# Kernel optimization log

Measured on AMD Instinct MI355X. Metric: run time of the kernel, lower is better.

Reference implementation:

```python
import jax, jax.numpy as jnp
import numpy as np

GRAPH_SIZE = 512  # N: graph_size from init


def setup_inputs() -> dict:
    key = jax.random.key(0)
    k1, k2 = jax.random.split(key)
    B, N, C_IN, C_OUT = 128, GRAPH_SIZE, 128, 128
    # X packs [adjacency | features] along last dim, matching the torch forward
    X = jax.random.uniform(k1, (B, N, N + C_IN), dtype=jnp.float32)
    W = jax.random.normal(k2, (C_IN, C_OUT), dtype=jnp.float32)
    return {"X": X, "W": W}


def reference(X, W):
    N = GRAPH_SIZE
    A = X[:, :, :N]            # [B, N, N] dense adjacency
    feat = X[:, :, N:]         # [B, N, C_in]
    # D = diag(rowsum(A)); pinv(D).sqrt() == diag(1/sqrt(deg)) with 0 where deg==0
    deg = jnp.sum(A, axis=2)   # [B, N]
    d_inv_sqrt = jnp.where(deg > 0, 1.0 / jnp.sqrt(deg), 0.0)
    A_hat = A + jnp.eye(N, dtype=A.dtype)  # A + I
    # D^-1/2 @ A_hat @ D^-1/2 as elementwise row/col scaling (diag matmuls)
    A_norm = d_inv_sqrt[:, :, None] * A_hat * d_inv_sqrt[:, None, :]
    # relu(A_norm @ X @ W)
    h = jnp.einsum('bnm,bmf->bnf', A_norm, feat)
    out = jax.nn.relu(jnp.einsum('bnf,fo->bno', h, W))
    return jnp.concatenate([A, out], axis=2)  # [B, N, N + C_out]
```

## Files before the change

kernel.cpp:

```cpp
#include <hip/hip_runtime.h>
#include <stdint.h>

#define GS   512
#define CF   128
#define XROW 640
#define NB   128

typedef __attribute__((ext_vector_type(4))) float          f32x4;
typedef __attribute__((ext_vector_type(8))) short          s16x8;
typedef __attribute__((ext_vector_type(4))) unsigned short u16x4;
typedef __attribute__((ext_vector_type(8))) unsigned short u16x8;

__device__ __forceinline__ unsigned short f2bf(float f) {
    unsigned u = __builtin_bit_cast(unsigned, f);
    u = (u + 0x7fffu + ((u >> 16) & 1u)) >> 16;
    return (unsigned short)u;
}
__device__ __forceinline__ float bf2f(unsigned short h) {
    unsigned u = ((unsigned)h) << 16;
    return __builtin_bit_cast(float, u);
}
__device__ __forceinline__ void glds16(const void* g, void* l) {
    __builtin_amdgcn_global_load_lds(
        (const __attribute__((address_space(1))) void*)g,
        (__attribute__((address_space(3))) void*)l, 16, 0, 0);
}

__global__ __launch_bounds__(256) void k0_wt(const float* __restrict__ W,
                                             unsigned short* __restrict__ WTst) {
    const int e = blockIdx.x * 256 + threadIdx.x;
    const int j = e & 7, f = (e >> 3) & 127, q = e >> 10;
    const int c = (q >> 2) * 32 + (q & 3) * 8 + j;
    WTst[e] = f2bf(W[c * CF + f]);
}

__global__ __launch_bounds__(256) void k1_pre(const float* __restrict__ X,
                                              float* __restrict__ out,
                                              float* __restrict__ dis,
                                              unsigned short* __restrict__ Abf) {
    const int wv = threadIdx.x >> 6, l = threadIdx.x & 63;
    const int gbase = blockIdx.x << 3;
#pragma unroll
    for (int p = 0; p < 2; ++p) {
        const int gr = gbase + wv + (p << 2);
        const f32x4* rp = (const f32x4*)(X + (size_t)gr * XROW);
        f32x4* op = (f32x4*)(out + (size_t)gr * XROW);
        f32x4 v0 = rp[2 * l], v1 = rp[2 * l + 1];
        op[2 * l] = v0; op[2 * l + 1] = v1;
        u16x8 o;
        o[0] = f2bf(v0[0]); o[1] = f2bf(v0[1]); o[2] = f2bf(v0[2]); o[3] = f2bf(v0[3]);
        o[4] = f2bf(v1[0]); o[5] = f2bf(v1[1]); o[6] = f2bf(v1[2]); o[7] = f2bf(v1[3]);
        const int b = gr >> 9, n = gr & (GS - 1);
        const int rt = n >> 4, lr = n & 15;
        *(u16x8*)((char*)Abf + (((size_t)(b * 32 + rt)) << 14) + (l << 8) + (lr << 4)) = o;
        float s = (v0[0] + v0[1]) + (v0[2] + v0[3]) + (v1[0] + v1[1]) + (v1[2] + v1[3]);
#pragma unroll
        for (int off = 32; off; off >>= 1) s += __shfl_xor(s, off, 64);
        if (l == 0) dis[gr] = (s > 0.f) ? (1.f / sqrtf(s)) : 0.f;
    }
}

__global__ __launch_bounds__(256) void k2_featw(const float* __restrict__ X,
                                                const unsigned short* __restrict__ WTst,
                                                const float* __restrict__ dis,
                                                unsigned short* __restrict__ fwdT) {
    __shared__ __align__(16) float sf[64 * 128];
    __shared__ __align__(16) unsigned short swt[16384];
    const int t = threadIdx.x, l = t & 63, wv = t >> 6;
    const int m0 = blockIdx.x << 6;
    const int b = m0 >> 9, ml0 = m0 & (GS - 1);

    const char* fb = (const char*)(X + (size_t)m0 * XROW + GS);
    char* sfb = (char*)sf;
#pragma unroll
    for (int it = 0; it < 8; ++it) {
        int chunk = it * 256 + t;
        int row = chunk >> 5, c16 = chunk & 31;
        int c16s = c16 ^ (row & 7);
        glds16(fb + (size_t)row * (XROW * 4) + c16s * 16, sfb + it * 4096 + wv * 1024);
    }
#pragma unroll
    for (int it = 0; it < 8; ++it)
        glds16((const char*)WTst + it * 4096 + wv * 1024 + l * 16,
               (char*)swt + it * 4096 + wv * 1024);
    __syncthreads();

    const int wr = wv >> 1, wc = wv & 1, lr = l & 15, lk = l >> 4;
    f32x4 acc[2][4];
#pragma unroll
    for (int i = 0; i < 2; ++i)
#pragma unroll
        for (int j = 0; j < 4; ++j)
#pragma unroll
            for (int r = 0; r < 4; ++r) acc[i][j][r] = 0.f;

#pragma unroll
    for (int ks = 0; ks < 4; ++ks) {
        s16x8 af[2];
#pragma unroll
        for (int i = 0; i < 2; ++i) {
            int row = (wr << 5) + (i << 4) + lr;
            int cb = (ks << 3) + (lk << 1);
            int c0 = cb ^ (row & 7), c1 = (cb + 1) ^ (row & 7);
            f32x4 x0 = *(const f32x4*)&sf[row * 128 + (c0 << 2)];
            f32x4 x1 = *(const f32x4*)&sf[row * 128 + (c1 << 2)];
            s16x8 a;
            a[0] = f2bf(x0[0]); a[1] = f2bf(x0[1]); a[2] = f2bf(x0[2]); a[3] = f2bf(x0[3]);
            a[4] = f2bf(x1[0]); a[5] = f2bf(x1[1]); a[6] = f2bf(x1[2]); a[7] = f2bf(x1[3]);
            af[i] = a;
        }
#pragma unroll
        for (int j = 0; j < 4; ++j) {
            int f = (wc << 6) + (j << 4) + lr;
            s16x8 bfr = *(const s16x8*)&swt[((((ks << 2) | lk) << 7) | f) << 3];
#pragma unroll
            for (int i = 0; i < 2; ++i)
                acc[i][j] = __builtin_amdgcn_mfma_f32_16x16x32_bf16(af[i], bfr, acc[i][j], 0, 0, 0);
        }
    }

#pragma unroll
    for (int i = 0; i < 2; ++i) {
        int mr = (wr << 5) + (i << 4) + (lk << 2);
        f32x4 d4 = *(const f32x4*)&dis[m0 + mr];
        int mg = ml0 + mr;
        int ktm = mg >> 5, q3 = (mg >> 3) & 3, jm = mg & 7;
#pragma unroll
        for (int j = 0; j < 4; ++j) {
            int f = (wc << 6) + (j << 4) + lr;
            u16x4 o;
            o[0] = f2bf(d4[0] * acc[i][j][0]);
            o[1] = f2bf(d4[1] * acc[i][j][1]);
            o[2] = f2bf(d4[2] * acc[i][j][2]);
            o[3] = f2bf(d4[3] * acc[i][j][3]);
            *(u16x4*)((char*)fwdT + ((size_t)b << 17) + (((ktm << 2) | q3) << 11)
                      + (f << 4) + (jm << 1)) = o;
        }
    }
}

__global__ __launch_bounds__(256) void k3_gcn(const unsigned short* __restrict__ Abf,
                                              const float* __restrict__ dis,
                                              const unsigned short* __restrict__ fwdT,
                                              float* __restrict__ out) {
    __shared__ __align__(16) unsigned short sb[2][4096];
    const int t = threadIdx.x, l = t & 63, wv = t >> 6, lr = l & 15, lk = l >> 4;
    const int b = blockIdx.x >> 3, bm0 = (blockIdx.x & 7) << 6;
    const char* Bt = (const char*)fwdT + ((size_t)b << 17);
    const int rt = (bm0 >> 4) + wv;
    const char* Ab = (const char*)Abf + (((size_t)(b * 32 + rt)) << 14);

    auto stage = [&](int buf, int kt) {
#pragma unroll
        for (int it = 0; it < 2; ++it)
            glds16(Bt + (kt << 13) + it * 4096 + wv * 1024 + l * 16,
                   (char*)sb[buf] + it * 4096 + wv * 1024);
    };

    f32x4 acc[8];
#pragma unroll
    for (int j = 0; j < 8; ++j)
#pragma unroll
        for (int r = 0; r < 4; ++r) acc[j][r] = 0.f;

    stage(0, 0);
    s16x8 a = *(const s16x8*)(Ab + (l << 4));
    int cur = 0;
    for (int kt = 0; kt < 16; ++kt) {
        __syncthreads();
        if (kt < 15) stage(cur ^ 1, kt + 1);
        s16x8 an = a;
        if (kt < 15) an = *(const s16x8*)(Ab + ((kt + 1) << 10) + (l << 4));
#pragma unroll
        for (int j = 0; j < 8; ++j) {
            s16x8 bfr = *(const s16x8*)&sb[cur][(lk << 10) + (j << 7) + (lr << 3)];
            acc[j] = __builtin_amdgcn_mfma_f32_16x16x32_bf16(a, bfr, acc[j], 0, 0, 0);
        }
        a = an; cur ^= 1;
    }

    const int n0 = bm0 + (wv << 4) + (lk << 2);
    f32x4 d4 = *(const f32x4*)&dis[(b << 9) + n0];
    const int ktm = n0 >> 5, q3 = (n0 >> 3) & 3, jm = n0 & 7;
#pragma unroll
    for (int j = 0; j < 8; ++j) {
        int f = (j << 4) + lr;
        u16x4 fw = *(const u16x4*)(Bt + (((ktm << 2) | q3) << 11) + (f << 4) + (jm << 1));
        float* ob = out + ((size_t)(b * GS + n0)) * XROW + GS + f;
#pragma unroll
        for (int r = 0; r < 4; ++r) {
            float v = d4[r] * (acc[j][r] + bf2f(fw[r]));
            ob[(size_t)r * XROW] = v > 0.f ? v : 0.f;
        }
    }
}

extern "C" void kernel_launch(void* const* d_in, const int* in_sizes, int n_in,
                              void* d_out, int out_size, void* d_ws, size_t ws_size,
                              hipStream_t stream) {
    const float* X = (const float*)d_in[0];
    const float* W = (const float*)d_in[1];
    float* out = (float*)d_out;
    float*          dis  = (float*)d_ws;
    unsigned short* WTst = (unsigned short*)((char*)d_ws + 262144);
    unsigned short* fwdT = (unsigned short*)((char*)d_ws + 294912);
    unsigned short* Abf  = (unsigned short*)((char*)d_ws + 17072128);

    hipLaunchKernelGGL(k0_wt,   dim3(64),   dim3(256), 0, stream, W, WTst);
    hipLaunchKernelGGL(k1_pre,  dim3(NB * GS / 8),  dim3(256), 0, stream, X, out, dis, Abf);
    hipLaunchKernelGGL(k2_featw, dim3(NB * GS / 64), dim3(256), 0, stream, X, WTst, dis, fwdT);
    hipLaunchKernelGGL(k3_gcn,  dim3(NB * GS / 64), dim3(256), 0, stream, Abf, dis, fwdT, out);
}
```

Before: 357.3 us.

## Store bf16 adjacency row-major and process two K-tiles per barrier in GCN GEMM

The preprocessing kernel now writes the bf16 adjacency copy in plain row-major order instead of a 16-row tiled fragment layout. This makes its stores fully contiguous. The aggregation kernel now reads A fragments directly from row-major rows, stages twice as much of the feature matrix per double-buffer step, and runs 16 MFMAs per barrier instead of 8. It also raises wave priority around the MFMA block. The trade-off is that A fragment loads in the GEMM become strided across rows (64-byte runs per row), and the shared-memory footprint doubles.

```diff
diff --git a/kernel.cpp b/kernel.cpp
--- a/kernel.cpp
+++ b/kernel.cpp
@@ -50,9 +50,7 @@
         u16x8 o;
         o[0] = f2bf(v0[0]); o[1] = f2bf(v0[1]); o[2] = f2bf(v0[2]); o[3] = f2bf(v0[3]);
         o[4] = f2bf(v1[0]); o[5] = f2bf(v1[1]); o[6] = f2bf(v1[2]); o[7] = f2bf(v1[3]);
-        const int b = gr >> 9, n = gr & (GS - 1);
-        const int rt = n >> 4, lr = n & 15;
-        *(u16x8*)((char*)Abf + (((size_t)(b * 32 + rt)) << 14) + (l << 8) + (lr << 4)) = o;
+        *(u16x8*)((char*)Abf + ((size_t)gr << 10) + (l << 4)) = o;
         float s = (v0[0] + v0[1]) + (v0[2] + v0[3]) + (v1[0] + v1[1]) + (v1[2] + v1[3]);
 #pragma unroll
         for (int off = 32; off; off >>= 1) s += __shfl_xor(s, off, 64);
@@ -143,17 +141,17 @@
                                               const float* __restrict__ dis,
                                               const unsigned short* __restrict__ fwdT,
                                               float* __restrict__ out) {
-    __shared__ __align__(16) unsigned short sb[2][4096];
+    __shared__ __align__(16) unsigned short sb[2][8192];
     const int t = threadIdx.x, l = t & 63, wv = t >> 6, lr = l & 15, lk = l >> 4;
     const int b = blockIdx.x >> 3, bm0 = (blockIdx.x & 7) << 6;
     const char* Bt = (const char*)fwdT + ((size_t)b << 17);
-    const int rt = (bm0 >> 4) + wv;
-    const char* Ab = (const char*)Abf + (((size_t)(b * 32 + rt)) << 14);
-
-    auto stage = [&](int buf, int kt) {
-#pragma unroll
-        for (int it = 0; it < 2; ++it)
-            glds16(Bt + (kt << 13) + it * 4096 + wv * 1024 + l * 16,
+    const char* Ab = (const char*)Abf
+        + (((size_t)(b * GS + bm0 + (wv << 4) + lr)) << 10) + (lk << 4);
+
+    auto stage = [&](int buf, int ph) {
+#pragma unroll
+        for (int it = 0; it < 4; ++it)
+            glds16(Bt + (ph << 14) + it * 4096 + wv * 1024 + l * 16,
                    (char*)sb[buf] + it * 4096 + wv * 1024);
     };
 
@@ -164,29 +162,40 @@
         for (int r = 0; r < 4; ++r) acc[j][r] = 0.f;
 
     stage(0, 0);
-    s16x8 a = *(const s16x8*)(Ab + (l << 4));
+    s16x8 a0 = *(const s16x8*)(Ab);
+    s16x8 a1 = *(const s16x8*)(Ab + 64);
     int cur = 0;
-    for (int kt = 0; kt < 16; ++kt) {
+    for (int ph = 0; ph < 8; ++ph) {
         __syncthreads();
-        if (kt < 15) stage(cur ^ 1, kt + 1);
-        s16x8 an = a;
-        if (kt < 15) an = *(const s16x8*)(Ab + ((kt + 1) << 10) + (l << 4));
+        if (ph < 7) stage(cur ^ 1, ph + 1);
+        s16x8 n0 = a0, n1 = a1;
+        if (ph < 7) {
+            n0 = *(const s16x8*)(Ab + ((2 * ph + 2) << 6));
+            n1 = *(const s16x8*)(Ab + ((2 * ph + 3) << 6));
+        }
+        __builtin_amdgcn_s_setprio(1);
 #pragma unroll
         for (int j = 0; j < 8; ++j) {
             s16x8 bfr = *(const s16x8*)&sb[cur][(lk << 10) + (j << 7) + (lr << 3)];
-            acc[j] = __builtin_amdgcn_mfma_f32_16x16x32_bf16(a, bfr, acc[j], 0, 0, 0);
-        }
-        a = an; cur ^= 1;
-    }
-
-    const int n0 = bm0 + (wv << 4) + (lk << 2);
-    f32x4 d4 = *(const f32x4*)&dis[(b << 9) + n0];
-    const int ktm = n0 >> 5, q3 = (n0 >> 3) & 3, jm = n0 & 7;
+            acc[j] = __builtin_amdgcn_mfma_f32_16x16x32_bf16(a0, bfr, acc[j], 0, 0, 0);
+        }
+#pragma unroll
+        for (int j = 0; j < 8; ++j) {
+            s16x8 bfr = *(const s16x8*)&sb[cur][4096 + (lk << 10) + (j << 7) + (lr << 3)];
+            acc[j] = __builtin_amdgcn_mfma_f32_16x16x32_bf16(a1, bfr, acc[j], 0, 0, 0);
+        }
+        __builtin_amdgcn_s_setprio(0);
+        a0 = n0; a1 = n1; cur ^= 1;
+    }
+
+    const int n0r = bm0 + (wv << 4) + (lk << 2);
+    f32x4 d4 = *(const f32x4*)&dis[(b << 9) + n0r];
+    const int ktm = n0r >> 5, q3 = (n0r >> 3) & 3, jm = n0r & 7;
 #pragma unroll
     for (int j = 0; j < 8; ++j) {
         int f = (j << 4) + lr;
         u16x4 fw = *(const u16x4*)(Bt + (((ktm << 2) | q3) << 11) + (f << 4) + (jm << 1));
-        float* ob = out + ((size_t)(b * GS + n0)) * XROW + GS + f;
+        float* ob = out + ((size_t)(b * GS + n0r)) * XROW + GS + f;
 #pragma unroll
         for (int r = 0; r < 4; ++r) {
             float v = d4[r] * (acc[j][r] + bf2f(fw[r]));
```

After: 335.4 us. -6.1%, faster.
